# Kernel tuning notes

Measured on AMD Instinct MI355X. Metric: run time of the kernel, lower is better.

Reference implementation:

```python
import jax, jax.numpy as jnp
import numpy as np

EPS = 1e-8

def mlp(x, w1, b1, w2, b2):
    return jnp.tanh(x @ w1 + b1) @ w2 + b2

def setup_inputs() -> dict:
    key = jax.random.key(0)
    ks = jax.random.split(key, 24)
    N_NEWS, N_USERS, N_ATR = 50000, 100000, 1000
    E_ATR, E_USR = 100000, 2000000
    D = 768
    def lin(k, fi, fo):
        return jax.random.normal(k, (fi, fo), jnp.float32) * (1.0 / np.sqrt(fi))
    inp = {
        'news_x': jax.random.normal(ks[0], (N_NEWS, D), jnp.float32),
        'users_x': jax.random.normal(ks[1], (N_USERS, 128), jnp.float32),
        'w1a': lin(ks[2], D, 256), 'b1a': jnp.zeros((256,), jnp.float32),
        'w1b': lin(ks[3], 256, 128), 'b1b': jnp.zeros((128,), jnp.float32),
        'wna': lin(ks[4], D + 128, 512), 'bna': jnp.zeros((512,), jnp.float32),
        'wnb': lin(ks[5], 512, 128), 'bnb': jnp.zeros((128,), jnp.float32),
        'wua': lin(ks[6], 256, 256), 'bua': jnp.zeros((256,), jnp.float32),
        'wub': lin(ks[7], 256, 128), 'bub': jnp.zeros((128,), jnp.float32),
        'atr_row': jax.random.randint(ks[8], (E_ATR,), 0, N_NEWS, jnp.int32),
        'atr_col': jax.random.randint(ks[9], (E_ATR,), 0, N_ATR, jnp.int32),
        'usr_row': jax.random.randint(ks[10], (E_USR,), 0, N_NEWS, jnp.int32),
        'usr_col': jax.random.randint(ks[11], (E_USR,), 0, N_USERS, jnp.int32),
        'n_news': N_NEWS, 'n_users': N_USERS, 'n_atr': N_ATR,
    }
    return inp

def reference(news_x, users_x, w1a, b1a, w1b, b1b, wna, bna, wnb, bnb,
              wua, bua, wub, bub, atr_row, atr_col, usr_row, usr_col,
              n_news, n_users, n_atr):
    dt = news_x.dtype
    ones_a = jnp.ones(atr_row.shape[0], dt)
    ones_u = jnp.ones(usr_row.shape[0], dt)
    # FirstConv: news -> attribute nodes (edge_index.t() @ news)
    deg_atr = jax.ops.segment_sum(ones_a, atr_col, num_segments=n_atr)
    agr_atr = jax.ops.segment_sum(news_x[atr_row], atr_col, num_segments=n_atr)
    agr_atr = agr_atr / (deg_atr[:, None] + EPS)
    atr_feats = mlp(agr_atr, w1a, b1a, w1b, b1b)  # [n_atr, 128]
    # NewsConv: attribute -> news (edge_index @ atr_feats), concat with news_x
    deg_news = jax.ops.segment_sum(ones_a, atr_row, num_segments=n_news)
    agr_news = jax.ops.segment_sum(atr_feats[atr_col], atr_row, num_segments=n_news)
    agr_news = agr_news / (deg_news[:, None] + EPS)
    news_out = mlp(jnp.concatenate([news_x, agr_news], axis=1), wna, bna, wnb, bnb)  # [n_news,128]
    # UserConv: news -> users (edge_index['users'].t() @ news), concat with users_x
    deg_usr = jax.ops.segment_sum(ones_u, usr_col, num_segments=n_users)
    agr_usr = jax.ops.segment_sum(news_out[usr_row], usr_col, num_segments=n_users)
    agr_usr = agr_usr / (deg_usr[:, None] + EPS)
    users_out = mlp(jnp.concatenate([users_x, agr_usr], axis=1), wua, bua, wub, bub)  # [n_users,128]
    # stack final news + user embeddings into one array
    return jnp.concatenate([news_out, users_out], axis=0)  # [n_news+n_users, 128]
```

## Files before the change

### kernel.cpp

```cpp
#include <hip/hip_runtime.h>

#define N_NEWS 50000
#define N_USERS 100000
#define N_ATR 1000
#define E_ATR 100000
#define E_USR 2000000
#define EPSF 1e-8f

#define ACAP 192
#define NCAP 24
#define P_USR 250
#define UPP 400
#define ACAPP 9216
#define EBLK_A 4096

typedef short s16x8 __attribute__((ext_vector_type(8)));
typedef float f32x4 __attribute__((ext_vector_type(4)));

__device__ inline ushort f2bf(float f) {
    uint u = __float_as_uint(f);
    u += 0x7fffu + ((u >> 16) & 1u);
    return (ushort)(u >> 16);
}
__device__ inline float bflo(uint v) { return __uint_as_float(v << 16); }
__device__ inline float bfhi(uint v) { return __uint_as_float(v & 0xffff0000u); }
__device__ inline float fast_tanh(float x) {
    x = fminf(fmaxf(x, -15.0f), 15.0f);
    float e = __expf(2.0f * x);
    return (e - 1.0f) / (e + 1.0f);
}

struct TrJob { const float* src; ushort* dst; int R, C, blkEnd; };

struct PrepArgs {
    const int *atr_row, *atr_col, *usr_row, *usr_col;
    int *cnt_atr, *cnt_news, *arena_cnt;
    int *ids_atr, *ids_news;
    unsigned long long* arena;
    const float *news_x, *users_x;
    ushort *news_bf, *users_bf;
    int pa, fa, tr, n1, n2;
    TrJob j[6];
};

__global__ void prep_k(PrepArgs A) {
    __shared__ float tile[32][33];
    __shared__ int cloc[256], cscn[256], sexc[256], cbase[256];
    __shared__ ushort stageI[EBLK_A];
    int b = blockIdx.x;
    int t = threadIdx.x;
    if (b < A.pa) {
        cloc[t] = 0;
        __syncthreads();
        int base = b * EBLK_A;
        int endE = base + EBLK_A; if (endE > E_USR) endE = E_USR;
        int n = endE - base;
        for (int e = base + t; e < endE; e += 256)
            atomicAdd(&cloc[A.usr_col[e] / UPP], 1);
        __syncthreads();
        cscn[t] = cloc[t];
        __syncthreads();
        for (int off = 1; off < 256; off <<= 1) {
            int v = (t >= off) ? cscn[t - off] : 0;
            __syncthreads();
            cscn[t] += v;
            __syncthreads();
        }
        sexc[t] = cscn[t] - cloc[t];
        if (t < P_USR) cbase[t] = atomicAdd(&A.arena_cnt[t], cloc[t]);
        cloc[t] = 0;
        __syncthreads();
        for (int e = base + t; e < endE; e += 256) {
            int p = A.usr_col[e] / UPP;
            int off = atomicAdd(&cloc[p], 1);
            stageI[sexc[p] + off] = (ushort)(e - base);
        }
        __syncthreads();
        for (int i = t; i < n; i += 256) {
            int e = base + stageI[i];
            int c = A.usr_col[e];
            int r = A.usr_row[e];
            int p = c / UPP;
            int dst = cbase[p] + (i - sexc[p]);
            if (dst < ACAPP)
                A.arena[(size_t)p * ACAPP + dst] =
                    ((unsigned long long)(uint)c << 32) | (uint)r;
        }
        return;
    }
    b -= A.pa;
    if (b < A.fa) {
        int total = 2 * E_ATR;
        int per = (total + A.fa - 1) / A.fa;
        int base = b * per;
        int endE = base + per; if (endE > total) endE = total;
        for (int e = base + t; e < endE; e += 256) {
            if (e < E_ATR) {
                int c = A.atr_col[e];
                int slot = atomicAdd(&A.cnt_atr[c], 1);
                if (slot < ACAP) A.ids_atr[(size_t)c * ACAP + slot] = A.atr_row[e];
            } else {
                int e2 = e - E_ATR;
                int r = A.atr_row[e2];
                int slot = atomicAdd(&A.cnt_news[r], 1);
                if (slot < NCAP) A.ids_news[(size_t)r * NCAP + slot] = A.atr_col[e2];
            }
        }
        return;
    }
    b -= A.fa;
    if (b < A.tr) {
        int ji = 0;
        while (b >= A.j[ji].blkEnd) ++ji;
        const TrJob& J = A.j[ji];
        int lb = b - (ji ? A.j[ji - 1].blkEnd : 0);
        int ctiles = J.C / 32;
        int bc = (lb % ctiles) * 32, br = (lb / ctiles) * 32;
        int tx = t & 31, ty = t >> 5;
        for (int i = 0; i < 4; ++i)
            tile[ty + i * 8][tx] = J.src[(size_t)(br + ty + i * 8) * J.C + bc + tx];
        __syncthreads();
        for (int i = 0; i < 4; ++i)
            J.dst[(size_t)(bc + ty + i * 8) * J.R + br + tx] = f2bf(tile[tx][ty + i * 8]);
        return;
    }
    b -= A.tr;
    int i = b * 256 + t;
    const float* src; ushort* dst;
    if (i < A.n1) { src = A.news_x; dst = A.news_bf; }
    else          { i -= A.n1; if (i >= A.n2) return; src = A.users_x; dst = A.users_bf; }
    float4 a = ((const float4*)src)[i];
    uint2 v;
    v.x = (uint)f2bf(a.x) | ((uint)f2bf(a.y) << 16);
    v.y = (uint)f2bf(a.z) | ((uint)f2bf(a.w) << 16);
    ((uint2*)dst)[i] = v;
}

struct MidArgs {
    const unsigned long long* arena;
    const int* arena_cnt;
    int *cnt_usr, *start_usr, *ids_usr;
    const ushort* news_bf;
    const int* ids_atr;
    const int* cnt_atr;
    ushort* agr_atr_b;
};

__global__ void mid_k(MidArgs M) {
    __shared__ int cnt[512];
    __shared__ int scn[512];
    int b = blockIdx.x;
    int t = threadIdx.x;
    if (b < P_USR) {
        int p = b;
        int nA = M.arena_cnt[p]; if (nA > ACAPP) nA = ACAPP;
        const unsigned long long* ar = M.arena + (size_t)p * ACAPP;
        cnt[t] = 0; cnt[t + 256] = 0;
        __syncthreads();
        for (int i = t; i < nA; i += 256)
            atomicAdd(&cnt[(int)(ar[i] >> 32) - p * UPP], 1);
        __syncthreads();
        scn[t] = cnt[t]; scn[t + 256] = cnt[t + 256];
        __syncthreads();
        for (int off = 1; off < 512; off <<= 1) {
            int v0 = (t >= off) ? scn[t - off] : 0;
            int v1 = ((t + 256) >= off) ? scn[t + 256 - off] : 0;
            __syncthreads();
            scn[t] += v0; scn[t + 256] += v1;
            __syncthreads();
        }
        for (int i = t; i < UPP; i += 256) {
            int u = p * UPP + i;
            M.cnt_usr[u] = cnt[i];
            M.start_usr[u] = p * ACAPP + (scn[i] - cnt[i]);
        }
        __syncthreads();
        for (int i = t; i < UPP; i += 256) cnt[i] = scn[i] - cnt[i];
        __syncthreads();
        for (int i = t; i < nA; i += 256) {
            unsigned long long v = ar[i];
            int c = (int)(v >> 32);
            int off = atomicAdd(&cnt[c - p * UPP], 1);
            M.ids_usr[(size_t)p * ACAPP + off] = (int)(v & 0xffffffffu);
        }
        return;
    }
    b -= P_USR;
    int u = b;
    int dc = M.cnt_atr[u];
    int d = dc < ACAP ? dc : ACAP;
    const int* bp = M.ids_atr + (size_t)u * ACAP;
    const ushort* src = M.news_bf;
    float a0 = 0.f, a1 = 0.f, a2 = 0.f, a3 = 0.f;
    int i = 0;
    for (; i + 3 < d; i += 4) {
        const uint* r0 = (const uint*)(src + (size_t)bp[i] * 768);
        const uint* r1 = (const uint*)(src + (size_t)bp[i + 1] * 768);
        const uint* r2 = (const uint*)(src + (size_t)bp[i + 2] * 768);
        const uint* r3 = (const uint*)(src + (size_t)bp[i + 3] * 768);
        uint v0 = r0[t], v1 = r1[t], v2 = r2[t], v3 = r3[t];
        a0 += bflo(v0) + bflo(v1) + bflo(v2) + bflo(v3);
        a1 += bfhi(v0) + bfhi(v1) + bfhi(v2) + bfhi(v3);
        if (t < 128) {
            uint w0 = r0[t + 256], w1 = r1[t + 256], w2 = r2[t + 256], w3 = r3[t + 256];
            a2 += bflo(w0) + bflo(w1) + bflo(w2) + bflo(w3);
            a3 += bfhi(w0) + bfhi(w1) + bfhi(w2) + bfhi(w3);
        }
    }
    for (; i < d; ++i) {
        const uint* r0 = (const uint*)(src + (size_t)bp[i] * 768);
        uint v0 = r0[t];
        a0 += bflo(v0); a1 += bfhi(v0);
        if (t < 128) {
            uint v1 = r0[t + 256];
            a2 += bflo(v1); a3 += bfhi(v1);
        }
    }
    float inv = 1.0f / ((float)dc + EPSF);
    uint* dst = (uint*)(M.agr_atr_b + (size_t)u * 768);
    dst[t] = (uint)f2bf(a0 * inv) | ((uint)f2bf(a1 * inv) << 16);
    if (t < 128)
        dst[256 + t] = (uint)f2bf(a2 * inv) | ((uint)f2bf(a3 * inv) << 16);
}

template<int CAP>
__global__ void gather128c_k(const ushort* __restrict__ srcp, const int* __restrict__ ids,
                             const int* __restrict__ cnt, ushort* __restrict__ agr, int n) {
    int u = blockIdx.x * 8 + (threadIdx.x >> 5);
    if (u >= n) return;
    int lane = threadIdx.x & 31;
    int dc = cnt[u];
    int d = dc < CAP ? dc : CAP;
    const int* bp = ids + (size_t)u * CAP;
    float a0 = 0.f, a1 = 0.f, a2 = 0.f, a3 = 0.f;
    int i = 0;
    for (; i + 3 < d; i += 4) {
        int s0 = bp[i], s1 = bp[i + 1], s2 = bp[i + 2], s3 = bp[i + 3];
        uint2 v0 = *((const uint2*)(srcp + (size_t)s0 * 128) + lane);
        uint2 v1 = *((const uint2*)(srcp + (size_t)s1 * 128) + lane);
        uint2 v2 = *((const uint2*)(srcp + (size_t)s2 * 128) + lane);
        uint2 v3 = *((const uint2*)(srcp + (size_t)s3 * 128) + lane);
        a0 += bflo(v0.x) + bflo(v1.x) + bflo(v2.x) + bflo(v3.x);
        a1 += bfhi(v0.x) + bfhi(v1.x) + bfhi(v2.x) + bfhi(v3.x);
        a2 += bflo(v0.y) + bflo(v1.y) + bflo(v2.y) + bflo(v3.y);
        a3 += bfhi(v0.y) + bfhi(v1.y) + bfhi(v2.y) + bfhi(v3.y);
    }
    for (; i < d; ++i) {
        uint2 v0 = *((const uint2*)(srcp + (size_t)bp[i] * 128) + lane);
        a0 += bflo(v0.x); a1 += bfhi(v0.x);
        a2 += bflo(v0.y); a3 += bfhi(v0.y);
    }
    float inv = 1.0f / ((float)dc + EPSF);
    uint2 packed;
    packed.x = (uint)f2bf(a0 * inv) | ((uint)f2bf(a1 * inv) << 16);
    packed.y = (uint)f2bf(a2 * inv) | ((uint)f2bf(a3 * inv) << 16);
    *((uint2*)(agr + (size_t)u * 128) + lane) = packed;
}

__global__ void gather128s_k(const ushort* __restrict__ srcp, const int* __restrict__ ids,
                             const int* __restrict__ start, const int* __restrict__ cnt,
                             ushort* __restrict__ agr, int n) {
    int u = blockIdx.x * 8 + (threadIdx.x >> 5);
    if (u >= n) return;
    int lane = threadIdx.x & 31;
    int d = cnt[u];
    const int* bp = ids + start[u];
    float a0 = 0.f, a1 = 0.f, a2 = 0.f, a3 = 0.f;
    int i = 0;
    for (; i + 7 < d; i += 8) {
        uint2 v0 = *((const uint2*)(srcp + (size_t)bp[i] * 128) + lane);
        uint2 v1 = *((const uint2*)(srcp + (size_t)bp[i + 1] * 128) + lane);
        uint2 v2 = *((const uint2*)(srcp + (size_t)bp[i + 2] * 128) + lane);
        uint2 v3 = *((const uint2*)(srcp + (size_t)bp[i + 3] * 128) + lane);
        uint2 v4 = *((const uint2*)(srcp + (size_t)bp[i + 4] * 128) + lane);
        uint2 v5 = *((const uint2*)(srcp + (size_t)bp[i + 5] * 128) + lane);
        uint2 v6 = *((const uint2*)(srcp + (size_t)bp[i + 6] * 128) + lane);
        uint2 v7 = *((const uint2*)(srcp + (size_t)bp[i + 7] * 128) + lane);
        a0 += bflo(v0.x) + bflo(v1.x) + bflo(v2.x) + bflo(v3.x)
            + bflo(v4.x) + bflo(v5.x) + bflo(v6.x) + bflo(v7.x);
        a1 += bfhi(v0.x) + bfhi(v1.x) + bfhi(v2.x) + bfhi(v3.x)
            + bfhi(v4.x) + bfhi(v5.x) + bfhi(v6.x) + bfhi(v7.x);
        a2 += bflo(v0.y) + bflo(v1.y) + bflo(v2.y) + bflo(v3.y)
            + bflo(v4.y) + bflo(v5.y) + bflo(v6.y) + bflo(v7.y);
        a3 += bfhi(v0.y) + bfhi(v1.y) + bfhi(v2.y) + bfhi(v3.y)
            + bfhi(v4.y) + bfhi(v5.y) + bfhi(v6.y) + bfhi(v7.y);
    }
    for (; i < d; ++i) {
        uint2 v0 = *((const uint2*)(srcp + (size_t)bp[i] * 128) + lane);
        a0 += bflo(v0.x); a1 += bfhi(v0.x);
        a2 += bflo(v0.y); a3 += bfhi(v0.y);
    }
    float inv = 1.0f / ((float)d + EPSF);
    uint2 packed;
    packed.x = (uint)f2bf(a0 * inv) | ((uint)f2bf(a1 * inv) << 16);
    packed.y = (uint)f2bf(a2 * inv) | ((uint)f2bf(a3 * inv) << 16);
    *((uint2*)(agr + (size_t)u * 128) + lane) = packed;
}

template<int NS, int NS1, bool TANH, int OMODE, int GY>
__launch_bounds__(256, 3)
__global__ void gemm5_k(const ushort* __restrict__ A1, const ushort* __restrict__ A2,
                        const ushort* __restrict__ Bt, const float* __restrict__ bias,
                        float* __restrict__ outf, ushort* __restrict__ outb,
                        int M, int N) {
    __shared__ __align__(16) char lds[32768];
    const int t = threadIdx.x;
    const int w = t >> 6, l = t & 63, lr = l & 15, lk = l >> 4;
    const int wm = w >> 1, wn = w & 1;
    int nwg = gridDim.x;
    int q = nwg >> 3, r = nwg & 7;
    int xcd = blockIdx.x & 7, idx = blockIdx.x >> 3;
    int fid = (xcd < r) ? xcd * (q + 1) + idx : r * (q + 1) + (xcd - r) * q + idx;
    constexpr int LG = (GY == 4) ? 2 : (GY == 2) ? 1 : 0;
    const int row0 = (fid >> LG) * 128;
    const int col0 = (fid & (GY - 1)) * 128;
    constexpr int A1RB = NS1 * 128;
    constexpr int A2RB = (NS - NS1) * 128;
    constexpr int BRB = NS * 128;

    auto stage = [&](int s) {
        const char* abase; int arb, soff;
        if (s < NS1) { abase = (const char*)A1; arb = A1RB; soff = s * 128; }
        else         { abase = (const char*)A2; arb = A2RB; soff = (s - NS1) * 128; }
#pragma unroll
        for (int i = 0; i < 4; ++i) {
            int chunk = i * 256 + w * 64 + l;
            int row = chunk >> 3, sub = chunk & 7;
            int rg = row0 + row; if (rg >= M) rg = M - 1;
            const char* src = abase + (size_t)rg * arb + soff + ((sub * 16) ^ ((row & 7) << 4));
            __builtin_amdgcn_global_load_lds(
                (const __attribute__((address_space(1))) unsigned int*)src,
                (__attribute__((address_space(3))) unsigned int*)(lds + i * 4096 + w * 1024),
                16, 0, 0);
        }
#pragma unroll
        for (int i = 0; i < 4; ++i) {
            int chunk = i * 256 + w * 64 + l;
            int row = chunk >> 3, sub = chunk & 7;
            const char* src = (const char*)Bt + (size_t)(col0 + row) * BRB + s * 128
                              + ((sub * 16) ^ ((row & 7) << 4));
            __builtin_amdgcn_global_load_lds(
                (const __attribute__((address_space(1))) unsigned int*)src,
                (__attribute__((address_space(3))) unsigned int*)(lds + 16384 + i * 4096 + w * 1024),
                16, 0, 0);
        }
    };

    f32x4 acc[4][4];
#pragma unroll
    for (int i = 0; i < 4; ++i)
#pragma unroll
        for (int j = 0; j < 4; ++j) acc[i][j] = (f32x4)0.f;

    stage(0);
    for (int s = 0; s < NS; ++s) {
        __syncthreads();
#pragma unroll
        for (int ks = 0; ks < 2; ++ks) {
            s16x8 af[4], bf[4];
#pragma unroll
            for (int rt = 0; rt < 4; ++rt) {
                int rr = wm * 64 + rt * 16 + lr;
                af[rt] = *(const s16x8*)(lds + rr * 128 + ((ks * 64 + lk * 16) ^ ((rr & 7) << 4)));
            }
#pragma unroll
            for (int ct = 0; ct < 4; ++ct) {
                int c = wn * 64 + ct * 16 + lr;
                bf[ct] = *(const s16x8*)(lds + 16384 + c * 128 + ((ks * 64 + lk * 16) ^ ((c & 7) << 4)));
            }
#pragma unroll
            for (int rt = 0; rt < 4; ++rt)
#pragma unroll
                for (int ct = 0; ct < 4; ++ct)
                    acc[rt][ct] = __builtin_amdgcn_mfma_f32_16x16x32_bf16(
                        af[rt], bf[ct], acc[rt][ct], 0, 0, 0);
        }
        __syncthreads();
        if (s + 1 < NS) stage(s + 1);
    }

    if (OMODE == 0) {
#pragma unroll
        for (int rt = 0; rt < 4; ++rt)
#pragma unroll
            for (int ct = 0; ct < 4; ++ct) {
                int c = wn * 64 + ct * 16 + lr;
                float bs = bias[col0 + c];
#pragma unroll
                for (int r4 = 0; r4 < 4; ++r4) {
                    int rr = wm * 64 + rt * 16 + lk * 4 + r4;
                    float v = acc[rt][ct][r4] + bs;
                    if (TANH) v = fast_tanh(v);
                    *(ushort*)(lds + rr * 256 + ((c * 2) ^ ((rr & 7) << 4))) = f2bf(v);
                }
            }
        __syncthreads();
#pragma unroll
        for (int i = 0; i < 8; ++i) {
            int chunk = i * 256 + t;
            int rr = chunk >> 4, cb = (chunk & 15) * 16;
            int rg = row0 + rr;
            if (rg < M)
                *(float4*)((char*)outb + (size_t)rg * (N * 2) + col0 * 2 + cb) =
                    *(const float4*)(lds + rr * 256 + (cb ^ ((rr & 7) << 4)));
        }
    } else {
#pragma unroll
        for (int rt = 0; rt < 4; ++rt)
#pragma unroll
            for (int ct = 0; ct < 4; ++ct) {
                int c = col0 + wn * 64 + ct * 16 + lr;
                float bs = bias[c];
#pragma unroll
                for (int r4 = 0; r4 < 4; ++r4) {
                    int rg = row0 + wm * 64 + rt * 16 + lk * 4 + r4;
                    if (rg < M) {
                        float v = acc[rt][ct][r4] + bs;
                        if (TANH) v = fast_tanh(v);
                        outf[(size_t)rg * N + c] = v;
                        if (OMODE == 2) outb[(size_t)rg * N + c] = f2bf(v);
                    }
                }
            }
    }
}

extern "C" void kernel_launch(void* const* d_in, const int* in_sizes, int n_in,
                              void* d_out, int out_size, void* d_ws, size_t ws_size,
                              hipStream_t stream) {
    const float* news_x  = (const float*)d_in[0];
    const float* users_x = (const float*)d_in[1];
    const float* w1a = (const float*)d_in[2];
    const float* b1a = (const float*)d_in[3];
    const float* w1b = (const float*)d_in[4];
    const float* b1b = (const float*)d_in[5];
    const float* wna = (const float*)d_in[6];
    const float* bna = (const float*)d_in[7];
    const float* wnb = (const float*)d_in[8];
    const float* bnb = (const float*)d_in[9];
    const float* wua = (const float*)d_in[10];
    const float* bua = (const float*)d_in[11];
    const float* wub = (const float*)d_in[12];
    const float* bub = (const float*)d_in[13];
    const int* atr_row = (const int*)d_in[14];
    const int* atr_col = (const int*)d_in[15];
    const int* usr_row = (const int*)d_in[16];
    const int* usr_col = (const int*)d_in[17];

    char* ws = (char*)d_ws;
    size_t o = 0;
    auto alloc = [&](size_t bytes) { void* p = ws + o; o += (bytes + 255) & ~(size_t)255; return p; };

    int* cnt_atr   = (int*)alloc(N_ATR * 4);
    int* cnt_news  = (int*)alloc(N_NEWS * 4);
    int* arena_cnt = (int*)alloc(P_USR * 4);
    size_t zero_bytes = o;
    int* cnt_usr   = (int*)alloc((size_t)N_USERS * 4);
    int* start_usr = (int*)alloc((size_t)N_USERS * 4);
    int* ids_atr  = (int*)alloc((size_t)N_ATR * ACAP * 4);
    int* ids_news = (int*)alloc((size_t)N_NEWS * NCAP * 4);
    int* ids_usr  = (int*)alloc((size_t)P_USR * ACAPP * 4);
    unsigned long long* arena = (unsigned long long*)alloc((size_t)P_USR * ACAPP * 8);
    ushort* news_bf    = (ushort*)alloc((size_t)N_NEWS * 768 * 2);
    ushort* users_bf   = (ushort*)alloc((size_t)N_USERS * 128 * 2);
    ushort* agr_atr_b  = (ushort*)alloc((size_t)N_ATR * 768 * 2);
    ushort* h_atr_b    = (ushort*)alloc((size_t)N_ATR * 256 * 2);
    ushort* atr_feats_b= (ushort*)alloc((size_t)N_ATR * 128 * 2);
    ushort* agr_news_b = (ushort*)alloc((size_t)N_NEWS * 128 * 2);
    ushort* agr_usr_b  = (ushort*)alloc((size_t)N_USERS * 128 * 2);
    ushort* out_news_b = (ushort*)alloc((size_t)N_NEWS * 128 * 2);
    ushort* h_buf      = (ushort*)alloc((size_t)N_USERS * 256 * 2);
    ushort* w1at = (ushort*)alloc((size_t)256 * 768 * 2);
    ushort* w1bt = (ushort*)alloc((size_t)128 * 256 * 2);
    ushort* wnat = (ushort*)alloc((size_t)512 * 896 * 2);
    ushort* wnbt = (ushort*)alloc((size_t)128 * 512 * 2);
    ushort* wuat = (ushort*)alloc((size_t)256 * 256 * 2);
    ushort* wubt = (ushort*)alloc((size_t)128 * 256 * 2);

    float* out = (float*)d_out;
    float* out_users = out + (size_t)N_NEWS * 128;

    hipMemsetAsync(cnt_atr, 0, zero_bytes, stream);

    {
        PrepArgs A;
        A.atr_row = atr_row; A.atr_col = atr_col;
        A.usr_row = usr_row; A.usr_col = usr_col;
        A.cnt_atr = cnt_atr; A.cnt_news = cnt_news; A.arena_cnt = arena_cnt;
        A.ids_atr = ids_atr; A.ids_news = ids_news;
        A.arena = arena;
        A.news_x = news_x; A.users_x = users_x;
        A.news_bf = news_bf; A.users_bf = users_bf;
        A.pa = (E_USR + EBLK_A - 1) / EBLK_A;
        A.fa = 25;
        A.n1 = N_NEWS * 768 / 4;
        A.n2 = N_USERS * 128 / 4;
        int acc2 = 0;
        auto add = [&](int i, const float* s, ushort* d, int R, int C) {
            acc2 += (C / 32) * (R / 32);
            A.j[i] = TrJob{s, d, R, C, acc2};
        };
        add(0, w1a, w1at, 768, 256);
        add(1, w1b, w1bt, 256, 128);
        add(2, wna, wnat, 896, 512);
        add(3, wnb, wnbt, 512, 128);
        add(4, wua, wuat, 256, 256);
        add(5, wub, wubt, 256, 128);
        A.tr = acc2;
        int cvt_blk = (A.n1 + A.n2 + 255) / 256;
        prep_k<<<A.pa + A.fa + A.tr + cvt_blk, 256, 0, stream>>>(A);
    }

    {
        MidArgs M;
        M.arena = arena; M.arena_cnt = arena_cnt;
        M.cnt_usr = cnt_usr; M.start_usr = start_usr; M.ids_usr = ids_usr;
        M.news_bf = news_bf; M.ids_atr = ids_atr; M.cnt_atr = cnt_atr;
        M.agr_atr_b = agr_atr_b;
        mid_k<<<P_USR + N_ATR, 256, 0, stream>>>(M);
    }

    gemm5_k<12, 12, true, 0, 2><<<16, 256, 0, stream>>>(
        agr_atr_b, nullptr, w1at, b1a, nullptr, h_atr_b, N_ATR, 256);
    gemm5_k<4, 4, false, 0, 1><<<8, 256, 0, stream>>>(
        h_atr_b, nullptr, w1bt, b1b, nullptr, atr_feats_b, N_ATR, 128);
    gather128c_k<NCAP><<<(N_NEWS + 7) / 8, 256, 0, stream>>>(
        atr_feats_b, ids_news, cnt_news, agr_news_b, N_NEWS);

    gemm5_k<14, 12, true, 0, 4><<<391 * 4, 256, 0, stream>>>(
        news_bf, agr_news_b, wnat, bna, nullptr, h_buf, N_NEWS, 512);
    gemm5_k<8, 8, false, 2, 1><<<391, 256, 0, stream>>>(
        h_buf, nullptr, wnbt, bnb, out, out_news_b, N_NEWS, 128);

    gather128s_k<<<(N_USERS + 7) / 8, 256, 0, stream>>>(
        out_news_b, ids_usr, start_usr, cnt_usr, agr_usr_b, N_USERS);
    gemm5_k<4, 2, true, 0, 2><<<782 * 2, 256, 0, stream>>>(
        users_bf, agr_usr_b, wuat, bua, nullptr, h_buf, N_USERS, 256);
    gemm5_k<4, 4, false, 1, 1><<<782, 256, 0, stream>>>(
        h_buf, nullptr, wubt, bub, out_users, nullptr, N_USERS, 128);
}
```

Baseline: 404.8 us.

## Fuse fp32-to-bf16 input conversion into GEMM A-tile loads and attribute gather

Removes the separate bulk conversion of news_x and users_x to bf16 in the prep kernel. The GEMMs now read fp32 A tiles into registers (prefetched one stage ahead), convert them, and write swizzled bf16 into LDS. The attribute gather reads fp32 news rows directly. This saves a full write and re-read of the converted inputs, but the GEMMs now read twice the A bytes through register staging instead of async LDS loads, which may raise register pressure.

```diff
diff --git a/kernel.cpp b/kernel.cpp
--- a/kernel.cpp
+++ b/kernel.cpp
@@ -37,9 +37,7 @@
     int *cnt_atr, *cnt_news, *arena_cnt;
     int *ids_atr, *ids_news;
     unsigned long long* arena;
-    const float *news_x, *users_x;
-    ushort *news_bf, *users_bf;
-    int pa, fa, tr, n1, n2;
+    int pa, fa, tr;
     TrJob j[6];
 };
 
@@ -109,38 +107,25 @@
         return;
     }
     b -= A.fa;
-    if (b < A.tr) {
-        int ji = 0;
-        while (b >= A.j[ji].blkEnd) ++ji;
-        const TrJob& J = A.j[ji];
-        int lb = b - (ji ? A.j[ji - 1].blkEnd : 0);
-        int ctiles = J.C / 32;
-        int bc = (lb % ctiles) * 32, br = (lb / ctiles) * 32;
-        int tx = t & 31, ty = t >> 5;
-        for (int i = 0; i < 4; ++i)
-            tile[ty + i * 8][tx] = J.src[(size_t)(br + ty + i * 8) * J.C + bc + tx];
-        __syncthreads();
-        for (int i = 0; i < 4; ++i)
-            J.dst[(size_t)(bc + ty + i * 8) * J.R + br + tx] = f2bf(tile[tx][ty + i * 8]);
-        return;
-    }
-    b -= A.tr;
-    int i = b * 256 + t;
-    const float* src; ushort* dst;
-    if (i < A.n1) { src = A.news_x; dst = A.news_bf; }
-    else          { i -= A.n1; if (i >= A.n2) return; src = A.users_x; dst = A.users_bf; }
-    float4 a = ((const float4*)src)[i];
-    uint2 v;
-    v.x = (uint)f2bf(a.x) | ((uint)f2bf(a.y) << 16);
-    v.y = (uint)f2bf(a.z) | ((uint)f2bf(a.w) << 16);
-    ((uint2*)dst)[i] = v;
+    int ji = 0;
+    while (b >= A.j[ji].blkEnd) ++ji;
+    const TrJob& J = A.j[ji];
+    int lb = b - (ji ? A.j[ji - 1].blkEnd : 0);
+    int ctiles = J.C / 32;
+    int bc = (lb % ctiles) * 32, br = (lb / ctiles) * 32;
+    int tx = t & 31, ty = t >> 5;
+    for (int i = 0; i < 4; ++i)
+        tile[ty + i * 8][tx] = J.src[(size_t)(br + ty + i * 8) * J.C + bc + tx];
+    __syncthreads();
+    for (int i = 0; i < 4; ++i)
+        J.dst[(size_t)(bc + ty + i * 8) * J.R + br + tx] = f2bf(tile[tx][ty + i * 8]);
 }
 
 struct MidArgs {
     const unsigned long long* arena;
     const int* arena_cnt;
     int *cnt_usr, *start_usr, *ids_usr;
-    const ushort* news_bf;
+    const float* news_x;
     const int* ids_atr;
     const int* cnt_atr;
     ushort* agr_atr_b;
@@ -190,30 +175,29 @@
     int dc = M.cnt_atr[u];
     int d = dc < ACAP ? dc : ACAP;
     const int* bp = M.ids_atr + (size_t)u * ACAP;
-    const ushort* src = M.news_bf;
     float a0 = 0.f, a1 = 0.f, a2 = 0.f, a3 = 0.f;
     int i = 0;
     for (; i + 3 < d; i += 4) {
-        const uint* r0 = (const uint*)(src + (size_t)bp[i] * 768);
-        const uint* r1 = (const uint*)(src + (size_t)bp[i + 1] * 768);
-        const uint* r2 = (const uint*)(src + (size_t)bp[i + 2] * 768);
-        const uint* r3 = (const uint*)(src + (size_t)bp[i + 3] * 768);
-        uint v0 = r0[t], v1 = r1[t], v2 = r2[t], v3 = r3[t];
-        a0 += bflo(v0) + bflo(v1) + bflo(v2) + bflo(v3);
-        a1 += bfhi(v0) + bfhi(v1) + bfhi(v2) + bfhi(v3);
+        const float2* r0 = (const float2*)(M.news_x + (size_t)bp[i] * 768);
+        const float2* r1 = (const float2*)(M.news_x + (size_t)bp[i + 1] * 768);
+        const float2* r2 = (const float2*)(M.news_x + (size_t)bp[i + 2] * 768);
+        const float2* r3 = (const float2*)(M.news_x + (size_t)bp[i + 3] * 768);
+        float2 v0 = r0[t], v1 = r1[t], v2 = r2[t], v3 = r3[t];
+        a0 += v0.x + v1.x + v2.x + v3.x;
+        a1 += v0.y + v1.y + v2.y + v3.y;
         if (t < 128) {
-            uint w0 = r0[t + 256], w1 = r1[t + 256], w2 = r2[t + 256], w3 = r3[t + 256];
-            a2 += bflo(w0) + bflo(w1) + bflo(w2) + bflo(w3);
-            a3 += bfhi(w0) + bfhi(w1) + bfhi(w2) + bfhi(w3);
+            float2 w0 = r0[256 + t], w1 = r1[256 + t], w2 = r2[256 + t], w3 = r3[256 + t];
+            a2 += w0.x + w1.x + w2.x + w3.x;
+            a3 += w0.y + w1.y + w2.y + w3.y;
         }
     }
     for (; i < d; ++i) {
-        const uint* r0 = (const uint*)(src + (size_t)bp[i] * 768);
-        uint v0 = r0[t];
-        a0 += bflo(v0); a1 += bfhi(v0);
+        const float2* r0 = (const float2*)(M.news_x + (size_t)bp[i] * 768);
+        float2 v0 = r0[t];
+        a0 += v0.x; a1 += v0.y;
         if (t < 128) {
-            uint v1 = r0[t + 256];
-            a2 += bflo(v1); a3 += bfhi(v1);
+            float2 w0 = r0[256 + t];
+            a2 += w0.x; a3 += w0.y;
         }
     }
     float inv = 1.0f / ((float)dc + EPSF);
@@ -297,7 +281,7 @@
     *((uint2*)(agr + (size_t)u * 128) + lane) = packed;
 }
 
-template<int NS, int NS1, bool TANH, int OMODE, int GY>
+template<int NS, int NS1, bool TANH, int OMODE, int GY, bool A1F32>
 __launch_bounds__(256, 3)
 __global__ void gemm5_k(const ushort* __restrict__ A1, const ushort* __restrict__ A2,
                         const ushort* __restrict__ Bt, const float* __restrict__ bias,
@@ -318,7 +302,30 @@
     constexpr int A2RB = (NS - NS1) * 128;
     constexpr int BRB = NS * 128;
 
-    auto stage = [&](int s) {
+    float4 sreg[8];
+
+    auto ldA = [&](int s) {
+        const float* Af = (const float*)A1;
+#pragma unroll
+        for (int i = 0; i < 8; ++i) {
+            int chunk = i * 256 + t;
+            int row = chunk >> 4, f4 = chunk & 15;
+            int rg = row0 + row; if (rg >= M) rg = M - 1;
+            sreg[i] = ((const float4*)(Af + (size_t)rg * (NS1 * 64) + s * 64))[f4];
+        }
+    };
+    auto writeA = [&]() {
+#pragma unroll
+        for (int i = 0; i < 8; ++i) {
+            int chunk = i * 256 + t;
+            int row = chunk >> 4, f4 = chunk & 15;
+            uint2 v;
+            v.x = (uint)f2bf(sreg[i].x) | ((uint)f2bf(sreg[i].y) << 16);
+            v.y = (uint)f2bf(sreg[i].z) | ((uint)f2bf(sreg[i].w) << 16);
+            *(uint2*)(lds + row * 128 + ((f4 * 8) ^ ((row & 7) << 4))) = v;
+        }
+    };
+    auto stageA_bf = [&](int s) {
         const char* abase; int arb, soff;
         if (s < NS1) { abase = (const char*)A1; arb = A1RB; soff = s * 128; }
         else         { abase = (const char*)A2; arb = A2RB; soff = (s - NS1) * 128; }
@@ -333,6 +340,8 @@
                 (__attribute__((address_space(3))) unsigned int*)(lds + i * 4096 + w * 1024),
                 16, 0, 0);
         }
+    };
+    auto stageB = [&](int s) {
 #pragma unroll
         for (int i = 0; i < 4; ++i) {
             int chunk = i * 256 + w * 64 + l;
@@ -352,9 +361,14 @@
 #pragma unroll
         for (int j = 0; j < 4; ++j) acc[i][j] = (f32x4)0.f;
 
-    stage(0);
+    if (A1F32 && NS1 > 0) { ldA(0); writeA(); }
+    else stageA_bf(0);
+    stageB(0);
+
     for (int s = 0; s < NS; ++s) {
         __syncthreads();
+        bool nxtF = A1F32 && (s + 1 < NS1);
+        if (nxtF) ldA(s + 1);
 #pragma unroll
         for (int ks = 0; ks < 2; ++ks) {
             s16x8 af[4], bf[4];
@@ -376,7 +390,11 @@
                         af[rt], bf[ct], acc[rt][ct], 0, 0, 0);
         }
         __syncthreads();
-        if (s + 1 < NS) stage(s + 1);
+        if (s + 1 < NS) {
+            if (nxtF) writeA();
+            else stageA_bf(s + 1);
+            stageB(s + 1);
+        }
     }
 
     if (OMODE == 0) {
@@ -461,8 +479,6 @@
     int* ids_news = (int*)alloc((size_t)N_NEWS * NCAP * 4);
     int* ids_usr  = (int*)alloc((size_t)P_USR * ACAPP * 4);
     unsigned long long* arena = (unsigned long long*)alloc((size_t)P_USR * ACAPP * 8);
-    ushort* news_bf    = (ushort*)alloc((size_t)N_NEWS * 768 * 2);
-    ushort* users_bf   = (ushort*)alloc((size_t)N_USERS * 128 * 2);
     ushort* agr_atr_b  = (ushort*)alloc((size_t)N_ATR * 768 * 2);
     ushort* h_atr_b    = (ushort*)alloc((size_t)N_ATR * 256 * 2);
     ushort* atr_feats_b= (ushort*)alloc((size_t)N_ATR * 128 * 2);
@@ -489,12 +505,8 @@
         A.cnt_atr = cnt_atr; A.cnt_news = cnt_news; A.arena_cnt = arena_cnt;
         A.ids_atr = ids_atr; A.ids_news = ids_news;
         A.arena = arena;
-        A.news_x = news_x; A.users_x = users_x;
-        A.news_bf = news_bf; A.users_bf = users_bf;
         A.pa = (E_USR + EBLK_A - 1) / EBLK_A;
         A.fa = 25;
-        A.n1 = N_NEWS * 768 / 4;
-        A.n2 = N_USERS * 128 / 4;
         int acc2 = 0;
         auto add = [&](int i, const float* s, ushort* d, int R, int C) {
             acc2 += (C / 32) * (R / 32);
@@ -507,35 +519,34 @@
         add(4, wua, wuat, 256, 256);
         add(5, wub, wubt, 256, 128);
         A.tr = acc2;
-        int cvt_blk = (A.n1 + A.n2 + 255) / 256;
-        prep_k<<<A.pa + A.fa + A.tr + cvt_blk, 256, 0, stream>>>(A);
+        prep_k<<<A.pa + A.fa + A.tr, 256, 0, stream>>>(A);
     }
 
     {
         MidArgs M;
         M.arena = arena; M.arena_cnt = arena_cnt;
         M.cnt_usr = cnt_usr; M.start_usr = start_usr; M.ids_usr = ids_usr;
-        M.news_bf = news_bf; M.ids_atr = ids_atr; M.cnt_atr = cnt_atr;
+        M.news_x = news_x; M.ids_atr = ids_atr; M.cnt_atr = cnt_atr;
         M.agr_atr_b = agr_atr_b;
         mid_k<<<P_USR + N_ATR, 256, 0, stream>>>(M);
     }
 
-    gemm5_k<12, 12, true, 0, 2><<<16, 256, 0, stream>>>(
+    gemm5_k<12, 12, true, 0, 2, false><<<16, 256, 0, stream>>>(
         agr_atr_b, nullptr, w1at, b1a, nullptr, h_atr_b, N_ATR, 256);
-    gemm5_k<4, 4, false, 0, 1><<<8, 256, 0, stream>>>(
+    gemm5_k<4, 4, false, 0, 1, false><<<8, 256, 0, stream>>>(
         h_atr_b, nullptr, w1bt, b1b, nullptr, atr_feats_b, N_ATR, 128);
     gather128c_k<NCAP><<<(N_NEWS + 7) / 8, 256, 0, stream>>>(
         atr_feats_b, ids_news, cnt_news, agr_news_b, N_NEWS);
 
-    gemm5_k<14, 12, true, 0, 4><<<391 * 4, 256, 0, stream>>>(
-        news_bf, agr_news_b, wnat, bna, nullptr, h_buf, N_NEWS, 512);
-    gemm5_k<8, 8, false, 2, 1><<<391, 256, 0, stream>>>(
+    gemm5_k<14, 12, true, 0, 4, true><<<391 * 4, 256, 0, stream>>>(
+        (const ushort*)news_x, agr_news_b, wnat, bna, nullptr, h_buf, N_NEWS, 512);
+    gemm5_k<8, 8, false, 2, 1, false><<<391, 256, 0, stream>>>(
         h_buf, nullptr, wnbt, bnb, out, out_news_b, N_NEWS, 128);
 
     gather128s_k<<<(N_USERS + 7) / 8, 256, 0, stream>>>(
         out_news_b, ids_usr, start_usr, cnt_usr, agr_usr_b, N_USERS);
-    gemm5_k<4, 2, true, 0, 2><<<782 * 2, 256, 0, stream>>>(
-        users_bf, agr_usr_b, wuat, bua, nullptr, h_buf, N_USERS, 256);
-    gemm5_k<4, 4, false, 1, 1><<<782, 256, 0, stream>>>(
+    gemm5_k<4, 2, true, 0, 2, true><<<782 * 2, 256, 0, stream>>>(
+        (const ushort*)users_x, agr_usr_b, wuat, bua, nullptr, h_buf, N_USERS, 256);
+    gemm5_k<4, 4, false, 1, 1, false><<<782, 256, 0, stream>>>(
         h_buf, nullptr, wubt, bub, out_users, nullptr, N_USERS, 128);
 }
```

Result: slower. 537.1 us (+32.7%).
